# Kernel optimization log

Hardware: AMD Instinct MI355X
Metric: run time of the kernel (lower is better)

## Reference

```python
import jax, jax.numpy as jnp
import numpy as np

N_NODES = 500_000
N_HYPER = 5_000_000
N_ADJ = 16_000_000


def setup_inputs() -> dict:
    key = jax.random.key(0)
    k1, k2, k3 = jax.random.split(key, 3)
    x = jax.random.uniform(k1, (N_NODES,), dtype=jnp.float32)
    hyper_edges = jax.random.randint(k2, (N_HYPER, 3), 0, N_NODES, dtype=jnp.int32)
    adj_edges = jax.random.randint(k3, (N_ADJ, 2), 0, N_NODES, dtype=jnp.int32)
    return {"x": x, "t": 0, "hyper_edges": hyper_edges, "adj_edges": adj_edges}


def reference(x, t, hyper_edges, adj_edges):
    # x: [N] node states; hyper_edges: [E,3] size-3 hyperedges; adj_edges: [M,2] (src,dst)
    N = x.shape[0]

    # --- hyperedge gather-product-scatter (update_result_3, vectorized) ---
    xe = x[hyper_edges]                       # [E,3] gathered member states
    prod = xe[:, 1] * xe[:, 2]                # product over nodes[1:]
    vals = prod[:, None] - xe * xe            # [E,3] per-member contribution
    hyper_res = jax.ops.segment_sum(
        vals.reshape(-1), hyper_edges.reshape(-1), num_segments=N)

    # --- sparse Laplacian SpMV: L@x = deg*x - A@x (edge-list form) ---
    src = adj_edges[:, 0]
    dst = adj_edges[:, 1]
    Ax = jax.ops.segment_sum(x[src], dst, num_segments=N)
    deg = jax.ops.segment_sum(jnp.ones_like(src, dtype=x.dtype), dst, num_segments=N)
    Lx = deg * x - Ax

    # forward: -0.1 * L@x + 0.9 * hyperedge result
    return -0.1 * Lx + 0.9 * hyper_res
```

## Files before the change

kernel.cpp:

```cpp
#include <hip/hip_runtime.h>
#include <hip/hip_fp16.h>


#define W_BUCKET   8192
#define W_SHIFT    13
#define NB_MAX     62
#define S_STAGE    128
#define A_THREADS  512
#define A_BLOCKS   1024
#define ADJ_TILE   4096
#define HYP_TILE   1536
#define B_PB       16
#define CAP_BUCKET 540672


__global__ __launch_bounds__(256) void zero_f4_kernel(float4* __restrict__ p, long long n4) {
    long long tid = (long long)blockIdx.x * blockDim.x + threadIdx.x;
    long long stride = (long long)gridDim.x * blockDim.x;
    for (long long i = tid; i < n4; i += stride) p[i] = make_float4(0.f, 0.f, 0.f, 0.f);
}

__global__ __launch_bounds__(256) void fused_scatter_kernel(
    const float* __restrict__ x, const int2* __restrict__ adj,
    const int* __restrict__ hyper, float* __restrict__ out,
    int n_adj, int n_hyper)
{
    const long long tid = (long long)blockIdx.x * blockDim.x + threadIdx.x;
    const long long stride = (long long)gridDim.x * blockDim.x;
    for (long long i = tid; i < n_adj; i += stride) {
        int2 e = adj[i];
        atomicAdd(&out[e.y], 0.1f * (x[e.x] - x[e.y]));
    }
    for (long long i = tid; i < n_hyper; i += stride) {
        int i0 = hyper[3*i], i1 = hyper[3*i+1], i2 = hyper[3*i+2];
        float x0 = x[i0], x1 = x[i1], x2 = x[i2];
        float p = x1 * x2;
        atomicAdd(&out[i0], 0.9f * (p - x0*x0));
        atomicAdd(&out[i1], 0.9f * (p - x1*x1));
        atomicAdd(&out[i2], 0.9f * (p - x2*x2));
    }
}


__global__ __launch_bounds__(256) void zero_int_kernel(int* __restrict__ p, int n) {
    int tid = blockIdx.x * blockDim.x + threadIdx.x;
    int stride = gridDim.x * blockDim.x;
    for (int i = tid; i < n; i += stride) p[i] = 0;
}


__device__ __forceinline__ unsigned int enc_rec(int dst, float v) {
    return ((unsigned int)(dst & (W_BUCKET - 1)) << 16)
         | (unsigned int)__half_as_ushort(__float2half(v));
}

__device__ __forceinline__ void stage_put(int b, int pos, int dst, float v,
                                          unsigned int* stage,
                                          float* __restrict__ g_direct) {
    if (pos < S_STAGE) stage[b * S_STAGE + pos] = enc_rec(dst, v);
    else atomicAdd(&g_direct[dst], v);
}

__device__ __forceinline__ void flush_stage(int nb, int* cur, int* basev, int* cnts,
                                            unsigned int* stage,
                                            int* __restrict__ g_cursor,
                                            unsigned int* __restrict__ g_records,
                                            float* __restrict__ g_direct,
                                            int wave, int lane, int nwaves) {
    __syncthreads();
    if (wave == 0 && lane < nb) {
        int c = min(cur[lane], S_STAGE);
        cur[lane] = 0;
        int base = 0;
        if (c > 0) base = atomicAdd(&g_cursor[lane], c);
        basev[lane] = base;
        cnts[lane]  = c;
    }
    __syncthreads();
    for (int b = wave; b < nb; b += nwaves) {
        int c = cnts[b];
        long long base = basev[b];
        for (int r = lane; r < c; r += 64) {
            long long idx = base + r;
            unsigned int rec = stage[b * S_STAGE + r];
            if (idx < CAP_BUCKET) {
                g_records[(long long)b * CAP_BUCKET + idx] = rec;
            } else {
                float v = __half2float(__ushort_as_half((unsigned short)(rec & 0xffffu)));
                atomicAdd(&g_direct[b * W_BUCKET + (int)(rec >> 16)], v);
            }
        }
    }
    __syncthreads();
}

__global__ __launch_bounds__(A_THREADS) void binning_kernel(
    const float* __restrict__ x,
    const int*  __restrict__ adj_raw, int n_adj,
    const int*  __restrict__ hyper, int n_hyper,
    int* __restrict__ g_cursor,
    float* __restrict__ g_direct,
    unsigned int* __restrict__ g_records,
    int nb)
{
    __shared__ unsigned int stage[NB_MAX * S_STAGE];
    __shared__ int cur[NB_MAX];
    __shared__ int basev[NB_MAX];
    __shared__ int cnts[NB_MAX];

    const int tid = threadIdx.x;
    const int wave = tid >> 6;
    const int lane = tid & 63;
    const int nwaves = A_THREADS >> 6;

    for (int b = tid; b < nb; b += A_THREADS) cur[b] = 0;
    __syncthreads();

    {
        long long per_blk = ((n_adj + A_BLOCKS - 1) / A_BLOCKS + 7) & ~7LL;
        long long a0 = (long long)blockIdx.x * per_blk;
        long long a1 = min((long long)n_adj, a0 + per_blk);
        for (long long t0 = a0; t0 < a1; t0 += ADJ_TILE) {
            long long t1 = min(a1, t0 + ADJ_TILE);
            for (long long g = t0 + (long long)tid * 4; g < t1; g += (long long)A_THREADS * 4) {
                if (g + 4 <= t1) {
                    const int4* p4 = (const int4*)(adj_raw + 2 * g);
                    int4 ea = p4[0], eb = p4[1];
                    float v0 = 0.1f * (x[ea.x] - x[ea.y]);
                    float v1 = 0.1f * (x[ea.z] - x[ea.w]);
                    float v2 = 0.1f * (x[eb.x] - x[eb.y]);
                    float v3 = 0.1f * (x[eb.z] - x[eb.w]);
                    int b0 = ea.y >> W_SHIFT, b1 = ea.w >> W_SHIFT;
                    int b2 = eb.y >> W_SHIFT, b3 = eb.w >> W_SHIFT;
                    int p0 = atomicAdd(&cur[b0], 1);
                    int p1 = atomicAdd(&cur[b1], 1);
                    int p2 = atomicAdd(&cur[b2], 1);
                    int p3 = atomicAdd(&cur[b3], 1);
                    stage_put(b0, p0, ea.y, v0, stage, g_direct);
                    stage_put(b1, p1, ea.w, v1, stage, g_direct);
                    stage_put(b2, p2, eb.y, v2, stage, g_direct);
                    stage_put(b3, p3, eb.w, v3, stage, g_direct);
                } else {
                    for (long long i = g; i < t1; ++i) {
                        int s = adj_raw[2*i], d = adj_raw[2*i+1];
                        float v = 0.1f * (x[s] - x[d]);
                        int b = d >> W_SHIFT;
                        int p = atomicAdd(&cur[b], 1);
                        stage_put(b, p, d, v, stage, g_direct);
                    }
                }
            }
            flush_stage(nb, cur, basev, cnts, stage, g_cursor, g_records, g_direct,
                        wave, lane, nwaves);
        }
    }

    {
        long long per_blk = ((n_hyper + A_BLOCKS - 1) / A_BLOCKS + 7) & ~7LL;
        long long h0 = (long long)blockIdx.x * per_blk;
        long long h1 = min((long long)n_hyper, h0 + per_blk);
        for (long long t0 = h0; t0 < h1; t0 += HYP_TILE) {
            long long t1 = min(h1, t0 + HYP_TILE);
            for (long long g = t0 + (long long)tid * 4; g < t1; g += (long long)A_THREADS * 4) {
                if (g + 4 <= t1) {
                    const int4* p4 = (const int4*)(hyper + 3 * g);
                    int4 w0 = p4[0], w1 = p4[1], w2 = p4[2];
                    int idx[12] = { w0.x, w0.y, w0.z,  w0.w, w1.x, w1.y,
                                    w1.z, w1.w, w2.x,  w2.y, w2.z, w2.w };
                    float xv[12];
                    #pragma unroll
                    for (int k = 0; k < 12; ++k) xv[k] = x[idx[k]];
                    #pragma unroll
                    for (int e = 0; e < 4; ++e) {
                        float xa = xv[3*e], xb = xv[3*e+1], xc = xv[3*e+2];
                        float pr = xb * xc;
                        int ia = idx[3*e], ib = idx[3*e+1], ic = idx[3*e+2];
                        int ba = ia >> W_SHIFT, bb = ib >> W_SHIFT, bc = ic >> W_SHIFT;
                        int pa = atomicAdd(&cur[ba], 1);
                        int pb = atomicAdd(&cur[bb], 1);
                        int pc = atomicAdd(&cur[bc], 1);
                        stage_put(ba, pa, ia, 0.9f * (pr - xa*xa), stage, g_direct);
                        stage_put(bb, pb, ib, 0.9f * (pr - xb*xb), stage, g_direct);
                        stage_put(bc, pc, ic, 0.9f * (pr - xc*xc), stage, g_direct);
                    }
                } else {
                    for (long long i = g; i < t1; ++i) {
                        int i0 = hyper[3*i], i1 = hyper[3*i+1], i2 = hyper[3*i+2];
                        float x0 = x[i0], x1 = x[i1], x2 = x[i2];
                        float pr = x1 * x2;
                        int b0 = i0 >> W_SHIFT, b1 = i1 >> W_SHIFT, b2 = i2 >> W_SHIFT;
                        int p0 = atomicAdd(&cur[b0], 1);
                        int p1 = atomicAdd(&cur[b1], 1);
                        int p2 = atomicAdd(&cur[b2], 1);
                        stage_put(b0, p0, i0, 0.9f * (pr - x0*x0), stage, g_direct);
                        stage_put(b1, p1, i1, 0.9f * (pr - x1*x1), stage, g_direct);
                        stage_put(b2, p2, i2, 0.9f * (pr - x2*x2), stage, g_direct);
                    }
                }
            }
            flush_stage(nb, cur, basev, cnts, stage, g_cursor, g_records, g_direct,
                        wave, lane, nwaves);
        }
    }
}


__device__ __forceinline__ void acc_one(float* acc, unsigned int rec) {
    float v = __half2float(__ushort_as_half((unsigned short)(rec & 0xffffu)));
    unsafeAtomicAdd(&acc[rec >> 16], v);
}

__global__ __launch_bounds__(512) void accumulate_kernel(
    const unsigned int* __restrict__ g_records,
    const int*  __restrict__ g_cursor,
    float* __restrict__ partials)
{
    __shared__ float acc[W_BUCKET];
    const int b = blockIdx.x / B_PB;
    const int j = blockIdx.x % B_PB;

    for (int i = threadIdx.x; i < W_BUCKET; i += blockDim.x) acc[i] = 0.f;
    __syncthreads();

    long long cnt = min(g_cursor[b], CAP_BUCKET);
    long long g8  = (cnt + 7) >> 3;
    long long s8  = g8 * j / B_PB;
    long long e8  = g8 * (j + 1) / B_PB;
    const uint4* rec4 = (const uint4*)(g_records + (long long)b * CAP_BUCKET);

    for (long long i8 = s8 + threadIdx.x; i8 < e8; i8 += blockDim.x) {
        uint4 r0 = rec4[2*i8], r1 = rec4[2*i8 + 1];
        long long base = i8 << 3;
        if (base + 7 < cnt) {
            acc_one(acc, r0.x); acc_one(acc, r0.y); acc_one(acc, r0.z); acc_one(acc, r0.w);
            acc_one(acc, r1.x); acc_one(acc, r1.y); acc_one(acc, r1.z); acc_one(acc, r1.w);
        } else {
            if (base + 0 < cnt) acc_one(acc, r0.x);
            if (base + 1 < cnt) acc_one(acc, r0.y);
            if (base + 2 < cnt) acc_one(acc, r0.z);
            if (base + 3 < cnt) acc_one(acc, r0.w);
            if (base + 4 < cnt) acc_one(acc, r1.x);
            if (base + 5 < cnt) acc_one(acc, r1.y);
            if (base + 6 < cnt) acc_one(acc, r1.z);
            if (base + 7 < cnt) acc_one(acc, r1.w);
        }
    }
    __syncthreads();

    float* p = partials + (long long)blockIdx.x * W_BUCKET;
    for (int i = threadIdx.x; i < W_BUCKET; i += blockDim.x) p[i] = acc[i];
}


__global__ __launch_bounds__(256) void finalize_kernel(
    const float* __restrict__ partials,
    const float* __restrict__ g_direct,
    float* __restrict__ out, int n_nodes)
{
    int tid = blockIdx.x * blockDim.x + threadIdx.x;
    int stride = gridDim.x * blockDim.x;
    for (int n = tid; n < n_nodes; n += stride) {
        int b = n >> W_SHIFT, l = n & (W_BUCKET - 1);
        float s = g_direct[n];
        const float* p = partials + ((long long)b * B_PB) * W_BUCKET + l;
        #pragma unroll
        for (int j = 0; j < B_PB; ++j) s += p[(long long)j * W_BUCKET];
        out[n] = s;
    }
}


extern "C" void kernel_launch(void* const* d_in, const int* in_sizes, int n_in,
                              void* d_out, int out_size, void* d_ws, size_t ws_size,
                              hipStream_t stream) {
    const float* x     = (const float*)d_in[0];
    const int*   hyper = (const int*)d_in[2];
    const int*   adj   = (const int*)d_in[3];
    float*       out   = (float*)d_out;

    const int n_nodes = in_sizes[0];
    const int n_hyper = in_sizes[2] / 3;
    const int n_adj   = in_sizes[3] / 2;
    const int nb      = (n_nodes + W_BUCKET - 1) / W_BUCKET;

    const size_t off_cursor = 0;
    const size_t off_direct = 256;
    size_t off_rec = off_direct + (size_t)n_nodes * 4;
    off_rec = (off_rec + 255) & ~(size_t)255;
    const size_t rec_bytes  = (size_t)NB_MAX * CAP_BUCKET * 4;
    size_t off_part = off_rec + rec_bytes;
    off_part = (off_part + 255) & ~(size_t)255;
    const size_t part_bytes = (size_t)NB_MAX * B_PB * W_BUCKET * 4;
    const size_t need = off_part + part_bytes;

    if (nb <= NB_MAX && (n_nodes & 3) == 0 && ws_size >= need) {
        int*          g_cursor  = (int*)          ((char*)d_ws + off_cursor);
        float*        g_direct  = (float*)        ((char*)d_ws + off_direct);
        unsigned int* g_records = (unsigned int*) ((char*)d_ws + off_rec);
        float*        partials  = (float*)        ((char*)d_ws + off_part);

        zero_int_kernel<<<256, 256, 0, stream>>>((int*)d_ws, (int)(off_rec / 4));

        binning_kernel<<<A_BLOCKS, A_THREADS, 0, stream>>>(
            x, adj, n_adj, hyper, n_hyper, g_cursor, g_direct, g_records, nb);

        accumulate_kernel<<<nb * B_PB, 512, 0, stream>>>(g_records, g_cursor, partials);

        finalize_kernel<<<1024, 256, 0, stream>>>(partials, g_direct, out, n_nodes);
    } else {
        zero_f4_kernel<<<512, 256, 0, stream>>>((float4*)out, n_nodes / 4);
        fused_scatter_kernel<<<2048, 256, 0, stream>>>(x, (const int2*)adj, hyper, out,
                                                       n_adj, n_hyper);
    }
}
```

Baseline: 582.3 us.

## Defer adjacency x gathers to accumulate pass by binning src indices instead of values

Adjacency records now store the destination-local index plus the source node index, so the binning pass no longer gathers x[src] and x[dst] for each edge. The accumulate kernel caches the bucket's x values in shared memory as half precision and gathers x[src] when it reads the records, and hyperedge records move to a separate buffer with their own cursors. This takes the random x gathers out of the binning kernel, where they sat beside the staging atomics, and turns the x[dst] lookups into shared-memory reads. In exchange the random x[src] gathers now happen in the accumulate kernel, x[dst] is rounded to half precision, and the fast path requires at most 2^19 nodes.

```diff
diff --git a/kernel.cpp b/kernel.cpp
--- a/kernel.cpp
+++ b/kernel.cpp
@@ -11,7 +11,9 @@
 #define ADJ_TILE   4096
 #define HYP_TILE   1536
 #define B_PB       16
-#define CAP_BUCKET 540672
+#define CAP_A      262144
+#define CAP_H      245760
+#define SRC_MASK   0x7FFFFu
 
 
 __global__ __launch_bounds__(256) void zero_f4_kernel(float4* __restrict__ p, long long n4) {
@@ -49,22 +51,13 @@
 }
 
 
-__device__ __forceinline__ unsigned int enc_rec(int dst, float v) {
-    return ((unsigned int)(dst & (W_BUCKET - 1)) << 16)
-         | (unsigned int)__half_as_ushort(__float2half(v));
-}
-
-__device__ __forceinline__ void stage_put(int b, int pos, int dst, float v,
-                                          unsigned int* stage,
-                                          float* __restrict__ g_direct) {
-    if (pos < S_STAGE) stage[b * S_STAGE + pos] = enc_rec(dst, v);
-    else atomicAdd(&g_direct[dst], v);
-}
-
+template <int KIND>
 __device__ __forceinline__ void flush_stage(int nb, int* cur, int* basev, int* cnts,
                                             unsigned int* stage,
                                             int* __restrict__ g_cursor,
                                             unsigned int* __restrict__ g_records,
+                                            long long cap,
+                                            const float* __restrict__ x,
                                             float* __restrict__ g_direct,
                                             int wave, int lane, int nwaves) {
     __syncthreads();
@@ -83,8 +76,12 @@
         for (int r = lane; r < c; r += 64) {
             long long idx = base + r;
             unsigned int rec = stage[b * S_STAGE + r];
-            if (idx < CAP_BUCKET) {
-                g_records[(long long)b * CAP_BUCKET + idx] = rec;
+            if (idx < cap) {
+                g_records[(long long)b * cap + idx] = rec;
+            } else if (KIND == 0) {
+                int src = rec & SRC_MASK;
+                int dst = b * W_BUCKET + (int)(rec >> 19);
+                atomicAdd(&g_direct[dst], 0.1f * (x[src] - x[dst]));
             } else {
                 float v = __half2float(__ushort_as_half((unsigned short)(rec & 0xffffu)));
                 atomicAdd(&g_direct[b * W_BUCKET + (int)(rec >> 16)], v);
@@ -98,9 +95,10 @@
     const float* __restrict__ x,
     const int*  __restrict__ adj_raw, int n_adj,
     const int*  __restrict__ hyper, int n_hyper,
-    int* __restrict__ g_cursor,
+    int* __restrict__ cur_a, int* __restrict__ cur_h,
     float* __restrict__ g_direct,
-    unsigned int* __restrict__ g_records,
+    unsigned int* __restrict__ rec_a,
+    unsigned int* __restrict__ rec_h,
     int nb)
 {
     __shared__ unsigned int stage[NB_MAX * S_STAGE];
@@ -126,32 +124,34 @@
                 if (g + 4 <= t1) {
                     const int4* p4 = (const int4*)(adj_raw + 2 * g);
                     int4 ea = p4[0], eb = p4[1];
-                    float v0 = 0.1f * (x[ea.x] - x[ea.y]);
-                    float v1 = 0.1f * (x[ea.z] - x[ea.w]);
-                    float v2 = 0.1f * (x[eb.x] - x[eb.y]);
-                    float v3 = 0.1f * (x[eb.z] - x[eb.w]);
-                    int b0 = ea.y >> W_SHIFT, b1 = ea.w >> W_SHIFT;
-                    int b2 = eb.y >> W_SHIFT, b3 = eb.w >> W_SHIFT;
+                    int s0 = ea.x, d0 = ea.y,  s1 = ea.z, d1 = ea.w;
+                    int s2 = eb.x, d2 = eb.y,  s3 = eb.z, d3 = eb.w;
+                    int b0 = d0 >> W_SHIFT, b1 = d1 >> W_SHIFT;
+                    int b2 = d2 >> W_SHIFT, b3 = d3 >> W_SHIFT;
                     int p0 = atomicAdd(&cur[b0], 1);
                     int p1 = atomicAdd(&cur[b1], 1);
                     int p2 = atomicAdd(&cur[b2], 1);
                     int p3 = atomicAdd(&cur[b3], 1);
-                    stage_put(b0, p0, ea.y, v0, stage, g_direct);
-                    stage_put(b1, p1, ea.w, v1, stage, g_direct);
-                    stage_put(b2, p2, eb.y, v2, stage, g_direct);
-                    stage_put(b3, p3, eb.w, v3, stage, g_direct);
+                    if (p0 < S_STAGE) stage[b0*S_STAGE+p0] = ((unsigned)(d0 & (W_BUCKET-1)) << 19) | (unsigned)s0;
+                    else atomicAdd(&g_direct[d0], 0.1f * (x[s0] - x[d0]));
+                    if (p1 < S_STAGE) stage[b1*S_STAGE+p1] = ((unsigned)(d1 & (W_BUCKET-1)) << 19) | (unsigned)s1;
+                    else atomicAdd(&g_direct[d1], 0.1f * (x[s1] - x[d1]));
+                    if (p2 < S_STAGE) stage[b2*S_STAGE+p2] = ((unsigned)(d2 & (W_BUCKET-1)) << 19) | (unsigned)s2;
+                    else atomicAdd(&g_direct[d2], 0.1f * (x[s2] - x[d2]));
+                    if (p3 < S_STAGE) stage[b3*S_STAGE+p3] = ((unsigned)(d3 & (W_BUCKET-1)) << 19) | (unsigned)s3;
+                    else atomicAdd(&g_direct[d3], 0.1f * (x[s3] - x[d3]));
                 } else {
                     for (long long i = g; i < t1; ++i) {
                         int s = adj_raw[2*i], d = adj_raw[2*i+1];
-                        float v = 0.1f * (x[s] - x[d]);
                         int b = d >> W_SHIFT;
                         int p = atomicAdd(&cur[b], 1);
-                        stage_put(b, p, d, v, stage, g_direct);
+                        if (p < S_STAGE) stage[b*S_STAGE+p] = ((unsigned)(d & (W_BUCKET-1)) << 19) | (unsigned)s;
+                        else atomicAdd(&g_direct[d], 0.1f * (x[s] - x[d]));
                     }
                 }
             }
-            flush_stage(nb, cur, basev, cnts, stage, g_cursor, g_records, g_direct,
-                        wave, lane, nwaves);
+            flush_stage<0>(nb, cur, basev, cnts, stage, cur_a, rec_a, CAP_A,
+                           x, g_direct, wave, lane, nwaves);
         }
     }
 
@@ -179,9 +179,15 @@
                         int pa = atomicAdd(&cur[ba], 1);
                         int pb = atomicAdd(&cur[bb], 1);
                         int pc = atomicAdd(&cur[bc], 1);
-                        stage_put(ba, pa, ia, 0.9f * (pr - xa*xa), stage, g_direct);
-                        stage_put(bb, pb, ib, 0.9f * (pr - xb*xb), stage, g_direct);
-                        stage_put(bc, pc, ic, 0.9f * (pr - xc*xc), stage, g_direct);
+                        float va = 0.9f * (pr - xa*xa);
+                        float vb = 0.9f * (pr - xb*xb);
+                        float vc = 0.9f * (pr - xc*xc);
+                        if (pa < S_STAGE) stage[ba*S_STAGE+pa] = ((unsigned)(ia & (W_BUCKET-1)) << 16) | (unsigned)__half_as_ushort(__float2half(va));
+                        else atomicAdd(&g_direct[ia], va);
+                        if (pb < S_STAGE) stage[bb*S_STAGE+pb] = ((unsigned)(ib & (W_BUCKET-1)) << 16) | (unsigned)__half_as_ushort(__float2half(vb));
+                        else atomicAdd(&g_direct[ib], vb);
+                        if (pc < S_STAGE) stage[bc*S_STAGE+pc] = ((unsigned)(ic & (W_BUCKET-1)) << 16) | (unsigned)__half_as_ushort(__float2half(vc));
+                        else atomicAdd(&g_direct[ic], vc);
                     }
                 } else {
                     for (long long i = g; i < t1; ++i) {
@@ -192,63 +198,99 @@
                         int p0 = atomicAdd(&cur[b0], 1);
                         int p1 = atomicAdd(&cur[b1], 1);
                         int p2 = atomicAdd(&cur[b2], 1);
-                        stage_put(b0, p0, i0, 0.9f * (pr - x0*x0), stage, g_direct);
-                        stage_put(b1, p1, i1, 0.9f * (pr - x1*x1), stage, g_direct);
-                        stage_put(b2, p2, i2, 0.9f * (pr - x2*x2), stage, g_direct);
+                        float v0 = 0.9f * (pr - x0*x0);
+                        float v1 = 0.9f * (pr - x1*x1);
+                        float v2 = 0.9f * (pr - x2*x2);
+                        if (p0 < S_STAGE) stage[b0*S_STAGE+p0] = ((unsigned)(i0 & (W_BUCKET-1)) << 16) | (unsigned)__half_as_ushort(__float2half(v0));
+                        else atomicAdd(&g_direct[i0], v0);
+                        if (p1 < S_STAGE) stage[b1*S_STAGE+p1] = ((unsigned)(i1 & (W_BUCKET-1)) << 16) | (unsigned)__half_as_ushort(__float2half(v1));
+                        else atomicAdd(&g_direct[i1], v1);
+                        if (p2 < S_STAGE) stage[b2*S_STAGE+p2] = ((unsigned)(i2 & (W_BUCKET-1)) << 16) | (unsigned)__half_as_ushort(__float2half(v2));
+                        else atomicAdd(&g_direct[i2], v2);
                     }
                 }
             }
-            flush_stage(nb, cur, basev, cnts, stage, g_cursor, g_records, g_direct,
-                        wave, lane, nwaves);
-        }
-    }
-}
-
-
-__device__ __forceinline__ void acc_one(float* acc, unsigned int rec) {
-    float v = __half2float(__ushort_as_half((unsigned short)(rec & 0xffffu)));
-    unsafeAtomicAdd(&acc[rec >> 16], v);
-}
+            flush_stage<1>(nb, cur, basev, cnts, stage, cur_h, rec_h, CAP_H,
+                           x, g_direct, wave, lane, nwaves);
+        }
+    }
+}
+
 
 __global__ __launch_bounds__(512) void accumulate_kernel(
-    const unsigned int* __restrict__ g_records,
-    const int*  __restrict__ g_cursor,
-    float* __restrict__ partials)
+    const float* __restrict__ x,
+    const unsigned int* __restrict__ rec_a,
+    const unsigned int* __restrict__ rec_h,
+    const int* __restrict__ cur_a,
+    const int* __restrict__ cur_h,
+    float* __restrict__ partials, int n_nodes)
 {
-    __shared__ float acc[W_BUCKET];
+    __shared__ float  acc[W_BUCKET];
+    __shared__ __half xs[W_BUCKET];
     const int b = blockIdx.x / B_PB;
     const int j = blockIdx.x % B_PB;
-
-    for (int i = threadIdx.x; i < W_BUCKET; i += blockDim.x) acc[i] = 0.f;
-    __syncthreads();
-
-    long long cnt = min(g_cursor[b], CAP_BUCKET);
-    long long g8  = (cnt + 7) >> 3;
-    long long s8  = g8 * j / B_PB;
-    long long e8  = g8 * (j + 1) / B_PB;
-    const uint4* rec4 = (const uint4*)(g_records + (long long)b * CAP_BUCKET);
-
-    for (long long i8 = s8 + threadIdx.x; i8 < e8; i8 += blockDim.x) {
-        uint4 r0 = rec4[2*i8], r1 = rec4[2*i8 + 1];
-        long long base = i8 << 3;
-        if (base + 7 < cnt) {
-            acc_one(acc, r0.x); acc_one(acc, r0.y); acc_one(acc, r0.z); acc_one(acc, r0.w);
-            acc_one(acc, r1.x); acc_one(acc, r1.y); acc_one(acc, r1.z); acc_one(acc, r1.w);
-        } else {
-            if (base + 0 < cnt) acc_one(acc, r0.x);
-            if (base + 1 < cnt) acc_one(acc, r0.y);
-            if (base + 2 < cnt) acc_one(acc, r0.z);
-            if (base + 3 < cnt) acc_one(acc, r0.w);
-            if (base + 4 < cnt) acc_one(acc, r1.x);
-            if (base + 5 < cnt) acc_one(acc, r1.y);
-            if (base + 6 < cnt) acc_one(acc, r1.z);
-            if (base + 7 < cnt) acc_one(acc, r1.w);
+    const int base_node = b * W_BUCKET;
+
+    for (int i = threadIdx.x; i < W_BUCKET; i += 512) {
+        acc[i] = 0.f;
+        int n = base_node + i;
+        xs[i] = __float2half(n < n_nodes ? x[n] : 0.f);
+    }
+    __syncthreads();
+
+    {
+        long long cnt = min(cur_a[b], CAP_A);
+        long long g8 = (cnt + 7) >> 3;
+        long long s8 = g8 * j / B_PB, e8 = g8 * (j + 1) / B_PB;
+        const uint4* r4 = (const uint4*)(rec_a + (long long)b * CAP_A);
+        for (long long i8 = s8 + threadIdx.x; i8 < e8; i8 += 512) {
+            uint4 r0 = r4[2*i8], r1 = r4[2*i8 + 1];
+            long long base = i8 << 3;
+            unsigned rr[8] = { r0.x, r0.y, r0.z, r0.w, r1.x, r1.y, r1.z, r1.w };
+            if (base + 7 < cnt) {
+                float xv[8];
+                #pragma unroll
+                for (int k = 0; k < 8; ++k) xv[k] = x[rr[k] & SRC_MASK];
+                #pragma unroll
+                for (int k = 0; k < 8; ++k) {
+                    int dl = rr[k] >> 19;
+                    unsafeAtomicAdd(&acc[dl], 0.1f * (xv[k] - __half2float(xs[dl])));
+                }
+            } else {
+                #pragma unroll
+                for (int k = 0; k < 8; ++k) {
+                    if (base + k < cnt) {
+                        int dl = rr[k] >> 19;
+                        unsafeAtomicAdd(&acc[dl],
+                            0.1f * (x[rr[k] & SRC_MASK] - __half2float(xs[dl])));
+                    }
+                }
+            }
+        }
+    }
+
+    {
+        long long cnt = min(cur_h[b], CAP_H);
+        long long g8 = (cnt + 7) >> 3;
+        long long s8 = g8 * j / B_PB, e8 = g8 * (j + 1) / B_PB;
+        const uint4* r4 = (const uint4*)(rec_h + (long long)b * CAP_H);
+        for (long long i8 = s8 + threadIdx.x; i8 < e8; i8 += 512) {
+            uint4 r0 = r4[2*i8], r1 = r4[2*i8 + 1];
+            long long base = i8 << 3;
+            unsigned rr[8] = { r0.x, r0.y, r0.z, r0.w, r1.x, r1.y, r1.z, r1.w };
+            #pragma unroll
+            for (int k = 0; k < 8; ++k) {
+                if (base + k < cnt) {
+                    float v = __half2float(__ushort_as_half((unsigned short)(rr[k] & 0xffffu)));
+                    unsafeAtomicAdd(&acc[rr[k] >> 16], v);
+                }
+            }
         }
     }
     __syncthreads();
 
     float* p = partials + (long long)blockIdx.x * W_BUCKET;
-    for (int i = threadIdx.x; i < W_BUCKET; i += blockDim.x) p[i] = acc[i];
+    for (int i = threadIdx.x; i < W_BUCKET; i += 512) p[i] = acc[i];
 }
 
 
@@ -283,28 +325,33 @@
     const int n_adj   = in_sizes[3] / 2;
     const int nb      = (n_nodes + W_BUCKET - 1) / W_BUCKET;
 
-    const size_t off_cursor = 0;
-    const size_t off_direct = 256;
-    size_t off_rec = off_direct + (size_t)n_nodes * 4;
-    off_rec = (off_rec + 255) & ~(size_t)255;
-    const size_t rec_bytes  = (size_t)NB_MAX * CAP_BUCKET * 4;
-    size_t off_part = off_rec + rec_bytes;
+    const size_t off_cur    = 0;
+    const size_t off_direct = 512;
+    size_t off_ra = off_direct + (size_t)n_nodes * 4;
+    off_ra = (off_ra + 255) & ~(size_t)255;
+    const size_t ra_bytes = (size_t)NB_MAX * CAP_A * 4;
+    size_t off_rh = off_ra + ra_bytes;
+    const size_t rh_bytes = (size_t)NB_MAX * CAP_H * 4;
+    size_t off_part = off_rh + rh_bytes;
     off_part = (off_part + 255) & ~(size_t)255;
     const size_t part_bytes = (size_t)NB_MAX * B_PB * W_BUCKET * 4;
     const size_t need = off_part + part_bytes;
 
-    if (nb <= NB_MAX && (n_nodes & 3) == 0 && ws_size >= need) {
-        int*          g_cursor  = (int*)          ((char*)d_ws + off_cursor);
-        float*        g_direct  = (float*)        ((char*)d_ws + off_direct);
-        unsigned int* g_records = (unsigned int*) ((char*)d_ws + off_rec);
-        float*        partials  = (float*)        ((char*)d_ws + off_part);
-
-        zero_int_kernel<<<256, 256, 0, stream>>>((int*)d_ws, (int)(off_rec / 4));
+    if (nb <= NB_MAX && n_nodes <= (1 << 19) && (n_nodes & 3) == 0 && ws_size >= need) {
+        int*          cur_a    = (int*)          ((char*)d_ws + off_cur);
+        int*          cur_h    = (int*)          ((char*)d_ws + off_cur + 256);
+        float*        g_direct = (float*)        ((char*)d_ws + off_direct);
+        unsigned int* rec_a    = (unsigned int*) ((char*)d_ws + off_ra);
+        unsigned int* rec_h    = (unsigned int*) ((char*)d_ws + off_rh);
+        float*        partials = (float*)        ((char*)d_ws + off_part);
+
+        zero_int_kernel<<<256, 256, 0, stream>>>((int*)d_ws, (int)(off_ra / 4));
 
         binning_kernel<<<A_BLOCKS, A_THREADS, 0, stream>>>(
-            x, adj, n_adj, hyper, n_hyper, g_cursor, g_direct, g_records, nb);
-
-        accumulate_kernel<<<nb * B_PB, 512, 0, stream>>>(g_records, g_cursor, partials);
+            x, adj, n_adj, hyper, n_hyper, cur_a, cur_h, g_direct, rec_a, rec_h, nb);
+
+        accumulate_kernel<<<nb * B_PB, 512, 0, stream>>>(
+            x, rec_a, rec_h, cur_a, cur_h, partials, n_nodes);
 
         finalize_kernel<<<1024, 256, 0, stream>>>(partials, g_direct, out, n_nodes);
     } else {
```

Result: faster. 519.0 us (-10.9%).
